# Kernel tuning notes

Measured on AMD Instinct MI355X. Metric: run time of the kernel, lower is better.

The kernel has to match this reference:

```python
import jax, jax.numpy as jnp
import numpy as np

NUM_ATOM_TYPE = 120
NUM_CHIRALITY_TAG = 3
NUM_BOND_TYPE = 6
NUM_BOND_DIRECTION = 3
EMB_DIM = 300
FEAT_DIM = 256
NUM_LAYER = 5
NUM_GRAPHS = 2048
OUT_DIM = 2  # classification: output_dim(1) * 2
BN_EPS = 1e-5


def setup_inputs() -> dict:
    key = jax.random.key(0)
    ks = jax.random.split(key, 20)
    N, E = 100000, 200000
    x = jax.random.randint(ks[0], (N, 2), 0, 3, dtype=jnp.int64) if jax.config.jax_enable_x64 else jax.random.randint(ks[0], (N, 2), 0, 3, dtype=jnp.int32)
    edge_index = jax.random.randint(ks[1], (2, E), 0, N, dtype=x.dtype)
    edge_attr = jax.random.randint(ks[2], (E, 2), 0, 3, dtype=x.dtype)
    batch = jnp.sort(jax.random.randint(ks[3], (N,), 0, NUM_GRAPHS, dtype=x.dtype))
    f32 = jnp.float32
    return {
        'x': x, 'edge_index': edge_index, 'edge_attr': edge_attr, 'batch': batch,
        'x_emb1': jax.random.normal(ks[4], (NUM_ATOM_TYPE, EMB_DIM), f32) * 0.1,
        'x_emb2': jax.random.normal(ks[5], (NUM_CHIRALITY_TAG, EMB_DIM), f32) * 0.1,
        'conv_w': jax.random.normal(ks[6], (NUM_LAYER, EMB_DIM, EMB_DIM), f32) * (1.0 / np.sqrt(EMB_DIM)),
        'conv_b': jnp.zeros((NUM_LAYER, EMB_DIM), f32),
        'eemb1': jax.random.normal(ks[7], (NUM_LAYER, NUM_BOND_TYPE, 1), f32) * 0.1,
        'eemb2': jax.random.normal(ks[8], (NUM_LAYER, NUM_BOND_DIRECTION, 1), f32) * 0.1,
        'bn_gamma': jnp.ones((NUM_LAYER, EMB_DIM), f32),
        'bn_beta': jnp.zeros((NUM_LAYER, EMB_DIM), f32),
        'feat_w': jax.random.normal(ks[9], (EMB_DIM, FEAT_DIM), f32) * (1.0 / np.sqrt(EMB_DIM)),
        'feat_b': jnp.zeros((FEAT_DIM,), f32),
        'pred_w1': jax.random.normal(ks[10], (FEAT_DIM, FEAT_DIM // 2), f32) * (1.0 / np.sqrt(FEAT_DIM)),
        'pred_b1': jnp.zeros((FEAT_DIM // 2,), f32),
        'pred_w2': jax.random.normal(ks[11], (FEAT_DIM // 2, OUT_DIM), f32) * (1.0 / np.sqrt(FEAT_DIM // 2)),
        'pred_b2': jnp.zeros((OUT_DIM,), f32),
    }


def reference(x, edge_index, edge_attr, batch, x_emb1, x_emb2, conv_w, conv_b,
              eemb1, eemb2, bn_gamma, bn_beta, feat_w, feat_b,
              pred_w1, pred_b1, pred_w2, pred_b2):
    N = x.shape[0]
    # add self loops (same for every layer)
    loop = jnp.arange(N, dtype=edge_index.dtype)
    src = jnp.concatenate([edge_index[0], loop])            # [E+N]
    dst = jnp.concatenate([edge_index[1], loop])            # [E+N]
    # self-loop edge attr: bond type 4, direction 0
    ea0 = jnp.concatenate([edge_attr[:, 0], jnp.full((N,), 4, edge_attr.dtype)])
    ea1 = jnp.concatenate([edge_attr[:, 1], jnp.zeros((N,), edge_attr.dtype)])

    h = x_emb1[x[:, 0]] + x_emb2[x[:, 1]]                   # [N, emb_dim]
    for l in range(NUM_LAYER):
        e = eemb1[l][ea0] + eemb2[l][ea1]                   # [E+N, 1]
        hw = h @ conv_w[l]                                  # [N, emb_dim]
        msg = hw[src] + e                                   # gather + broadcast-add
        out = jax.ops.segment_sum(msg, dst, num_segments=N) + conv_b[l]
        # BatchNorm1d (training-mode batch stats, biased variance)
        mean = jnp.mean(out, axis=0)
        var = jnp.mean((out - mean) ** 2, axis=0)
        out = (out - mean) * jax.lax.rsqrt(var + BN_EPS) * bn_gamma[l] + bn_beta[l]
        h = jax.nn.relu(out)                                # dropout p=0

    h = h @ feat_w + feat_b                                 # [N, feat_dim]
    # global mean pool per graph
    sums = jax.ops.segment_sum(h, batch, num_segments=NUM_GRAPHS)
    counts = jax.ops.segment_sum(jnp.ones((N,), h.dtype), batch, num_segments=NUM_GRAPHS)
    g = sums / jnp.maximum(counts, 1.0)[:, None]            # [G, feat_dim]
    pred = jax.nn.relu(g @ pred_w1 + pred_b1) @ pred_w2 + pred_b2
    return (g, pred)
```

## Files before the change

### kernel.cpp

```cpp
#include <hip/hip_runtime.h>
#include <math.h>

#define EMB 300
#define KP 320
#define FEAT 256
#define NLAYER 5
#define NGRAPH 2048
#define BNEPS 1e-5f
#define SCAN_B 256
#define NPART 64
#define CH 40
#define CHW 20

typedef __attribute__((ext_vector_type(8))) short short8;
typedef __attribute__((ext_vector_type(8))) unsigned short ushort8;
typedef __attribute__((ext_vector_type(4))) float f32x4;

#define GLOAD_LDS16(src, dst) __builtin_amdgcn_global_load_lds( \
    (const __attribute__((address_space(1))) unsigned int*)(const void*)(src), \
    (__attribute__((address_space(3))) unsigned int*)(void*)(dst), 16, 0, 0)

static __device__ __forceinline__ unsigned short f2bf(float f) {
    unsigned int u = __float_as_uint(f);
    unsigned int r = (u + 0x7FFFu + ((u >> 16) & 1u)) >> 16;
    return (unsigned short)r;
}
static __device__ __forceinline__ float bf2f(unsigned short h) {
    return __uint_as_float(((unsigned int)h) << 16);
}

__global__ void k_prepW(const float* __restrict__ convw, const float* __restrict__ featw,
                        unsigned short* __restrict__ whi) {
    int idx = blockIdx.x * 256 + threadIdx.x;
    if (idx >= 1856 * KP) return;
    int row = idx / KP;
    int k = idx - row * KP;
    float w = 0.f;
    if (row < 1600) {
        int l = row / KP;
        int c = row - l * KP;
        if (c < EMB && k < EMB) w = convw[(size_t)l * EMB * EMB + (size_t)k * EMB + c];
    } else {
        int c = row - 1600;
        if (k < EMB) w = featw[(size_t)k * FEAT + c];
    }
    whi[idx] = f2bf(w);
}

__global__ void k_s_all(const int* __restrict__ ei, const int* __restrict__ ea,
                        const float* __restrict__ eemb1, const float* __restrict__ eemb2,
                        float* __restrict__ s, int N, int E) {
    int t = blockIdx.x * blockDim.x + threadIdx.x;
    int total = E + N;
    if (t >= total) return;
    if (t < E) {
        int d = ei[E + t];
        int a0 = ea[2 * t], a1 = ea[2 * t + 1];
        for (int l = 0; l < NLAYER; ++l) {
            float v = eemb1[l * 6 + a0] + eemb2[l * 3 + a1];
            atomicAdd(&s[(size_t)l * N + d], v);
        }
    } else {
        int v = t - E;
        for (int l = 0; l < NLAYER; ++l) {
            float val = eemb1[l * 6 + 4] + eemb2[l * 3 + 0];
            atomicAdd(&s[(size_t)l * N + v], val);
        }
    }
}

__global__ void k_count(const int* __restrict__ ei, int* __restrict__ deg, int E) {
    int e = blockIdx.x * blockDim.x + threadIdx.x;
    if (e < E) atomicAdd(&deg[ei[E + e]], 1);
}

__global__ void k_scanA(const int* __restrict__ deg, int* __restrict__ bsum, int N) {
    __shared__ int sm[SCAN_B];
    int i = blockIdx.x * SCAN_B + threadIdx.x;
    sm[threadIdx.x] = (i < N) ? deg[i] : 0;
    __syncthreads();
    for (int off = SCAN_B / 2; off > 0; off >>= 1) {
        if (threadIdx.x < off) sm[threadIdx.x] += sm[threadIdx.x + off];
        __syncthreads();
    }
    if (threadIdx.x == 0) bsum[blockIdx.x] = sm[0];
}

__global__ void k_scanB(int* __restrict__ bsum, int nb, int* __restrict__ rowptr, int N) {
    if (threadIdx.x == 0 && blockIdx.x == 0) {
        int acc = 0;
        for (int i = 0; i < nb; ++i) { int v = bsum[i]; bsum[i] = acc; acc += v; }
        rowptr[N] = acc;
    }
}

__global__ void k_scanC(const int* __restrict__ deg, const int* __restrict__ bsum,
                        int* __restrict__ rowptr, int N) {
    __shared__ int sm[SCAN_B];
    int i = blockIdx.x * SCAN_B + threadIdx.x;
    int v = (i < N) ? deg[i] : 0;
    sm[threadIdx.x] = v;
    __syncthreads();
    for (int off = 1; off < SCAN_B; off <<= 1) {
        int add = (threadIdx.x >= off) ? sm[threadIdx.x - off] : 0;
        __syncthreads();
        sm[threadIdx.x] += add;
        __syncthreads();
    }
    if (i < N) rowptr[i] = bsum[blockIdx.x] + sm[threadIdx.x] - v;
}

__global__ void k_scatter(const int* __restrict__ ei, const int* __restrict__ rowptr,
                          int* __restrict__ cursor, int* __restrict__ esrc, int E) {
    int e = blockIdx.x * blockDim.x + threadIdx.x;
    if (e >= E) return;
    int d = ei[E + e], srcv = ei[e];
    int p = atomicAdd(&cursor[d], 1);
    esrc[rowptr[d] + p] = srcv;
}

__global__ void k_h0(const int* __restrict__ x, const float* __restrict__ emb1,
                     const float* __restrict__ emb2, unsigned short* __restrict__ h0, int N) {
    int idx = blockIdx.x * 256 + threadIdx.x;
    if (idx >= N * 160) return;
    int v = idx / 160, fp = idx - v * 160;
    unsigned int out = 0;
    if (fp < 150) {
        int f = fp * 2;
        size_t b1 = (size_t)x[2 * v] * EMB + f;
        size_t b2 = (size_t)x[2 * v + 1] * EMB + f;
        float a = emb1[b1] + emb2[b2];
        float b = emb1[b1 + 1] + emb2[b2 + 1];
        out = (unsigned int)f2bf(a) | ((unsigned int)f2bf(b) << 16);
    }
    *(unsigned int*)(h0 + (size_t)v * KP + fp * 2) = out;
}

template <bool BN>
__global__ __launch_bounds__(256) void k_aggV(
    const unsigned short* __restrict__ Prev, const int* __restrict__ rowptr,
    const int* __restrict__ esrc,
    const float* __restrict__ scale, const float* __restrict__ shift,
    unsigned short* __restrict__ A, int N) {
    int idx = blockIdx.x * 256 + threadIdx.x;
    if (idx >= N * CHW) return;
    int row = idx / CHW, c = idx - row * CHW;
    int f0 = c * 16;

    f32x4 sc[4], sh[4];
    if constexpr (BN) {
#pragma unroll
        for (int g = 0; g < 4; ++g) {
            sc[g] = *(const f32x4*)(scale + f0 + g * 4);
            sh[g] = *(const f32x4*)(shift + f0 + g * 4);
        }
    }
    int rs = rowptr[row], re = rowptr[row + 1];

    float f[16];
    {
        const unsigned short* pr = Prev + (size_t)row * KP + f0;
        ushort8 u0 = *(const ushort8*)pr;
        ushort8 u1 = *(const ushort8*)(pr + 8);
#pragma unroll
        for (int e = 0; e < 8; ++e) {
            if constexpr (BN) {
                f[e]     = fmaxf(fmaf(bf2f(u0[e]), sc[e >> 2][e & 3], sh[e >> 2][e & 3]), 0.f);
                f[e + 8] = fmaxf(fmaf(bf2f(u1[e]), sc[2 + (e >> 2)][e & 3], sh[2 + (e >> 2)][e & 3]), 0.f);
            } else {
                f[e] = bf2f(u0[e]);
                f[e + 8] = bf2f(u1[e]);
            }
        }
    }
    int ii = rs;
    int un = (ii < re) ? esrc[ii] : 0;
    while (ii < re) {
        int ucur = un;
        ++ii;
        if (ii < re) un = esrc[ii];
        const unsigned short* pu = Prev + (size_t)ucur * KP + f0;
        ushort8 uu0 = *(const ushort8*)pu;
        ushort8 uu1 = *(const ushort8*)(pu + 8);
#pragma unroll
        for (int e = 0; e < 8; ++e) {
            if constexpr (BN) {
                f[e]     += fmaxf(fmaf(bf2f(uu0[e]), sc[e >> 2][e & 3], sh[e >> 2][e & 3]), 0.f);
                f[e + 8] += fmaxf(fmaf(bf2f(uu1[e]), sc[2 + (e >> 2)][e & 3], sh[2 + (e >> 2)][e & 3]), 0.f);
            } else {
                f[e] += bf2f(uu0[e]);
                f[e + 8] += bf2f(uu1[e]);
            }
        }
    }
    short8 v0, v1;
#pragma unroll
    for (int e = 0; e < 8; ++e) {
        v0[e] = (short)f2bf(f[e]);
        v1[e] = (short)f2bf(f[e + 8]);
    }
    unsigned short* dst = A + (size_t)row * KP + f0;
    *(short8*)dst = v0;
    *(short8*)(dst + 8) = v1;
}

template <int COLF, int BMT, bool BN>
__global__ __launch_bounds__(256, 2) void k_mm(
    const unsigned short* __restrict__ Prev,
    const float* __restrict__ scale, const float* __restrict__ shift,
    const unsigned short* __restrict__ Whi,
    const float* __restrict__ bias, const float* __restrict__ svec,
    unsigned short* __restrict__ OutB,
    float* __restrict__ partsum, float* __restrict__ partsq, int N) {
    __shared__ unsigned short As[BMT * KP];
    constexpr int WSTR = (COLF == 5) ? KP : FEAT;
    constexpr int RF = BMT / 16;
    constexpr int NCHUNK = BMT * CH;
    int tid = threadIdx.x;
    int row0 = blockIdx.x * BMT;
    int wave = tid >> 6, lane = tid & 63;

    if constexpr (!BN) {
#pragma unroll
        for (int it = 0; it < NCHUNK / 256; ++it) {
            int base = it * 256 + wave * 64;
            int idx = base + lane;
            int r = idx / CH, c = idx - r * CH;
            const unsigned short* src =
                Prev + (size_t)(row0 + r) * KP + (size_t)(c ^ (r & 7)) * 8;
            GLOAD_LDS16(src, &As[(size_t)base * 8]);
        }
    } else {
        for (int idx = tid; idx < NCHUNK; idx += 256) {
            int r = idx / CH, c = idx - r * CH;
            int row = row0 + r;
            short8 v = (short8){0, 0, 0, 0, 0, 0, 0, 0};
            if (row < N) {
                ushort8 u = *(const ushort8*)(Prev + (size_t)row * KP + c * 8);
                f32x4 s0 = *(const f32x4*)(scale + c * 8);
                f32x4 s1 = *(const f32x4*)(scale + c * 8 + 4);
                f32x4 t0 = *(const f32x4*)(shift + c * 8);
                f32x4 t1 = *(const f32x4*)(shift + c * 8 + 4);
#pragma unroll
                for (int e = 0; e < 4; ++e) {
                    v[e]     = (short)f2bf(fmaxf(fmaf(bf2f(u[e]), s0[e], t0[e]), 0.f));
                    v[e + 4] = (short)f2bf(fmaxf(fmaf(bf2f(u[e + 4]), s1[e], t1[e]), 0.f));
                }
            }
            *(short8*)&As[(size_t)(r * CH + (c ^ (r & 7))) * 8] = v;
        }
    }
    __syncthreads();

    int q = lane >> 4, m = lane & 15;
    int wbase = wave * (COLF * 16);

    f32x4 acc[RF][COLF];
#pragma unroll
    for (int rf = 0; rf < RF; ++rf)
#pragma unroll
        for (int cf = 0; cf < COLF; ++cf)
            acc[rf][cf] = (f32x4){0.f, 0.f, 0.f, 0.f};

    size_t woff[COLF];
#pragma unroll
    for (int cf = 0; cf < COLF; ++cf)
        woff[cf] = (size_t)(wbase + cf * 16 + m) * KP;

#pragma unroll 2
    for (int ks = 0; ks < 10; ++ks) {
        short8 a[RF];
#pragma unroll
        for (int rf = 0; rf < RF; ++rf) {
            int r = rf * 16 + m;
            int ch = ks * 4 + q;
            a[rf] = *(const short8*)&As[(size_t)(r * CH + (ch ^ (r & 7))) * 8];
        }
        int kb = ks * 32 + q * 8;
#pragma unroll
        for (int cf = 0; cf < COLF; ++cf) {
            short8 bh = *(const short8*)(Whi + woff[cf] + kb);
#pragma unroll
            for (int rf = 0; rf < RF; ++rf) {
                acc[rf][cf] = __builtin_amdgcn_mfma_f32_16x16x32_bf16(a[rf], bh, acc[rf][cf], 0, 0, 0);
            }
        }
    }

    __syncthreads();

    if constexpr (COLF == 5) {
        float sv[RF][4];
#pragma unroll
        for (int rf = 0; rf < RF; ++rf)
#pragma unroll
            for (int i = 0; i < 4; ++i) {
                int row = row0 + rf * 16 + q * 4 + i;
                sv[rf][i] = (row < N) ? svec[row] : 0.f;
            }
        int part = blockIdx.x & (NPART - 1);
#pragma unroll
        for (int cf = 0; cf < COLF; ++cf) {
            int col = wbase + cf * 16 + m;
            bool cok = col < EMB;
            float bia = cok ? bias[col] : 0.f;
            float lsum = 0.f, lsq = 0.f;
#pragma unroll
            for (int rf = 0; rf < RF; ++rf)
#pragma unroll
                for (int i = 0; i < 4; ++i) {
                    int r = rf * 16 + q * 4 + i;
                    int row = row0 + r;
                    float val = 0.f;
                    if (cok && row < N) {
                        val = acc[rf][cf][i] + bia + sv[rf][i];
                        lsum += val; lsq += val * val;
                    }
                    As[(size_t)r * WSTR + col] = f2bf(val);
                }
            lsum += __shfl_xor(lsum, 16); lsum += __shfl_xor(lsum, 32);
            lsq  += __shfl_xor(lsq, 16);  lsq  += __shfl_xor(lsq, 32);
            if (q == 0 && cok) {
                atomicAdd(&partsum[(size_t)part * KP + col], lsum);
                atomicAdd(&partsq[(size_t)part * KP + col], lsq);
            }
        }
    } else {
#pragma unroll
        for (int cf = 0; cf < COLF; ++cf) {
            int col = wbase + cf * 16 + m;
            float bia = bias[col];
#pragma unroll
            for (int rf = 0; rf < RF; ++rf)
#pragma unroll
                for (int i = 0; i < 4; ++i) {
                    int r = rf * 16 + q * 4 + i;
                    As[(size_t)r * WSTR + col] = f2bf(acc[rf][cf][i] + bia);
                }
        }
    }
    __syncthreads();

    unsigned short* dst = OutB + (size_t)row0 * WSTR;
    for (int idx = tid; idx < BMT * WSTR / 8; idx += 256) {
        *(short8*)(dst + (size_t)idx * 8) = *(const short8*)&As[(size_t)idx * 8];
    }
}

__global__ __launch_bounds__(64) void k_bnred(
    const float* __restrict__ partsum, const float* __restrict__ partsq,
    const float* __restrict__ gamma, const float* __restrict__ beta,
    float* __restrict__ scale, float* __restrict__ shift, int N) {
    int j = blockIdx.x;
    int p = threadIdx.x;
    if (j >= EMB) {
        if (p == 0) { scale[j] = 0.f; shift[j] = 0.f; }
        return;
    }
    float s = partsum[(size_t)p * KP + j];
    float sq = partsq[(size_t)p * KP + j];
#pragma unroll
    for (int off = 32; off > 0; off >>= 1) {
        s += __shfl_down(s, off);
        sq += __shfl_down(sq, off);
    }
    if (p == 0) {
        float invN = 1.0f / (float)N;
        float mean = s * invN;
        float var = sq * invN - mean * mean;
        float sc = gamma[j] * rsqrtf(var + BNEPS);
        scale[j] = sc;
        shift[j] = beta[j] - mean * sc;
    }
}

__global__ void k_counts(const int* __restrict__ batch, float* __restrict__ counts, int N) {
    int i = blockIdx.x * blockDim.x + threadIdx.x;
    if (i < N) atomicAdd(&counts[batch[i]], 1.0f);
}

#define PROWS 128
__global__ __launch_bounds__(256) void k_pool(const unsigned short* __restrict__ H,
                                              const int* __restrict__ batch,
                                              float* __restrict__ gsums, int N) {
    int j = threadIdx.x;
    int r0 = blockIdx.x * PROWS;
    int rend = min(r0 + PROWS, N);
    float run = 0.f;
    int curg = -1;
    for (int r = r0; r < rend; ++r) {
        int g = batch[r];
        if (g != curg) {
            if (curg >= 0) atomicAdd(&gsums[(size_t)curg * FEAT + j], run);
            curg = g; run = 0.f;
        }
        run += bf2f(H[(size_t)r * FEAT + j]);
    }
    if (curg >= 0) atomicAdd(&gsums[(size_t)curg * FEAT + j], run);
}

__global__ void k_poolfin(const float* __restrict__ gsums, const float* __restrict__ counts,
                          float* __restrict__ gout) {
    int i = blockIdx.x * blockDim.x + threadIdx.x;
    if (i >= NGRAPH * FEAT) return;
    int g = i / FEAT;
    gout[i] = gsums[i] / fmaxf(counts[g], 1.0f);
}

__global__ __launch_bounds__(128) void k_pred(
    const float* __restrict__ gout, const float* __restrict__ w1, const float* __restrict__ b1,
    const float* __restrict__ w2, const float* __restrict__ b2, float* __restrict__ pout) {
    __shared__ float gs[FEAT];
    __shared__ float h1[128];
    int g = blockIdx.x;
    for (int k = threadIdx.x; k < FEAT; k += 128) gs[k] = gout[(size_t)g * FEAT + k];
    __syncthreads();
    int j = threadIdx.x;
    float acc = b1[j];
    for (int k = 0; k < FEAT; ++k) acc = fmaf(gs[k], w1[(size_t)k * 128 + j], acc);
    h1[j] = fmaxf(acc, 0.f);
    __syncthreads();
    if (j < 2) {
        float acc2 = b2[j];
        for (int k = 0; k < 128; ++k) acc2 = fmaf(h1[k], w2[k * 2 + j], acc2);
        pout[(size_t)g * 2 + j] = acc2;
    }
}

extern "C" void kernel_launch(void* const* d_in, const int* in_sizes, int n_in,
                              void* d_out, int out_size, void* d_ws, size_t ws_size,
                              hipStream_t stream) {
    const int* x      = (const int*)d_in[0];
    const int* ei     = (const int*)d_in[1];
    const int* ea     = (const int*)d_in[2];
    const int* batch  = (const int*)d_in[3];
    const float* xemb1 = (const float*)d_in[4];
    const float* xemb2 = (const float*)d_in[5];
    const float* convw = (const float*)d_in[6];
    const float* convb = (const float*)d_in[7];
    const float* eemb1 = (const float*)d_in[8];
    const float* eemb2 = (const float*)d_in[9];
    const float* gamma = (const float*)d_in[10];
    const float* beta  = (const float*)d_in[11];
    const float* featw = (const float*)d_in[12];
    const float* featb = (const float*)d_in[13];
    const float* pw1   = (const float*)d_in[14];
    const float* pb1   = (const float*)d_in[15];
    const float* pw2   = (const float*)d_in[16];
    const float* pb2   = (const float*)d_in[17];

    int N = in_sizes[0] / 2;
    int E = in_sizes[1] / 2;
    int nrb = (N + 127) / 128;
    size_t Npad = (size_t)nrb * 128;

    char* p = (char*)d_ws;
    auto alloc = [&](size_t bytes) { char* r = p; p += (bytes + 255) & ~255ull; return r; };
    unsigned short* H0Hf = (unsigned short*)alloc(Npad * KP * 2);
    unsigned short* Abf  = (unsigned short*)alloc(Npad * KP * 2);
    unsigned short* OutB = (unsigned short*)alloc(Npad * KP * 2);
    float* sAll    = (float*)alloc((size_t)NLAYER * N * 4);
    float* partsum = (float*)alloc((size_t)NLAYER * NPART * KP * 4);
    float* partsq  = (float*)alloc((size_t)NLAYER * NPART * KP * 4);
    char*  zero1_end = p;
    float* scaleA  = (float*)alloc((size_t)NLAYER * KP * 4);
    float* shiftA  = (float*)alloc((size_t)NLAYER * KP * 4);
    unsigned short* Whi = (unsigned short*)alloc((size_t)1856 * KP * 2);
    int*   deg    = (int*)alloc((size_t)N * 4);
    int*   rowptr = (int*)alloc((size_t)(N + 1) * 4);
    int*   cursor = (int*)alloc((size_t)N * 4);
    char*  zero2_end = p;
    int*   esrc   = (int*)alloc((size_t)E * 4);
    float* gsums  = (float*)alloc((size_t)NGRAPH * FEAT * 4);
    float* counts = (float*)alloc(NGRAPH * 4);
    char*  zero3_end = p;
    int nb = (N + SCAN_B - 1) / SCAN_B;
    int*   bsum   = (int*)alloc((size_t)nb * 4);

    hipMemsetAsync(sAll, 0, (size_t)(zero1_end - (char*)sAll), stream);
    hipMemsetAsync(deg, 0, (size_t)(zero2_end - (char*)deg), stream);
    hipMemsetAsync(gsums, 0, (size_t)(zero3_end - (char*)gsums), stream);
    if (Npad > (size_t)N)
        hipMemsetAsync(Abf + (size_t)N * KP, 0, (Npad - (size_t)N) * KP * 2, stream);

    int tpb = 256;
    k_prepW<<<(1856 * KP + 255) / 256, 256, 0, stream>>>(convw, featw, Whi);
    k_s_all<<<(E + N + tpb - 1) / tpb, tpb, 0, stream>>>(ei, ea, eemb1, eemb2, sAll, N, E);
    k_count<<<(E + tpb - 1) / tpb, tpb, 0, stream>>>(ei, deg, E);
    k_scanA<<<nb, SCAN_B, 0, stream>>>(deg, bsum, N);
    k_scanB<<<1, 64, 0, stream>>>(bsum, nb, rowptr, N);
    k_scanC<<<nb, SCAN_B, 0, stream>>>(deg, bsum, rowptr, N);
    k_scatter<<<(E + tpb - 1) / tpb, tpb, 0, stream>>>(ei, rowptr, cursor, esrc, E);
    k_h0<<<(N * 160 + 255) / 256, 256, 0, stream>>>(x, xemb1, xemb2, H0Hf, N);

    int gagg = (N * CHW + 255) / 256;
    k_aggV<false><<<gagg, 256, 0, stream>>>(H0Hf, rowptr, esrc, nullptr, nullptr, Abf, N);

    for (int l = 0; l < NLAYER; ++l) {
        k_mm<5, 128, false><<<nrb, 256, 0, stream>>>(
            Abf, nullptr, nullptr,
            Whi + (size_t)l * KP * KP,
            convb + (size_t)l * EMB, sAll + (size_t)l * N,
            OutB,
            partsum + (size_t)l * NPART * KP, partsq + (size_t)l * NPART * KP, N);
        k_bnred<<<KP, 64, 0, stream>>>(
            partsum + (size_t)l * NPART * KP, partsq + (size_t)l * NPART * KP,
            gamma + (size_t)l * EMB, beta + (size_t)l * EMB,
            scaleA + (size_t)l * KP, shiftA + (size_t)l * KP, N);
        if (l < NLAYER - 1)
            k_aggV<true><<<gagg, 256, 0, stream>>>(OutB, rowptr, esrc,
                                                   scaleA + (size_t)l * KP, shiftA + (size_t)l * KP,
                                                   Abf, N);
    }

    k_mm<4, 128, true><<<nrb, 256, 0, stream>>>(
        OutB, scaleA + (size_t)4 * KP, shiftA + (size_t)4 * KP,
        Whi + (size_t)1600 * KP,
        featb, nullptr,
        H0Hf, nullptr, nullptr, N);

    float* gout = (float*)d_out;
    float* pout = gout + (size_t)NGRAPH * FEAT;
    k_counts<<<(N + tpb - 1) / tpb, tpb, 0, stream>>>(batch, counts, N);
    k_pool<<<(N + PROWS - 1) / PROWS, 256, 0, stream>>>(H0Hf, batch, gsums, N);
    k_poolfin<<<(NGRAPH * FEAT + tpb - 1) / tpb, tpb, 0, stream>>>(gsums, counts, gout);
    k_pred<<<NGRAPH, 128, 0, stream>>>(gout, pw1, pb1, pw2, pb2, pout);
}
```

Before: 811.0 us.

## Replace per-layer edge-embedding atomics with attribute histogram and fold pooling kernels

Measured after the change: 745.7 us. -8.0%, faster.

```diff
diff --git a/kernel.cpp b/kernel.cpp
--- a/kernel.cpp
+++ b/kernel.cpp
@@ -47,25 +47,30 @@
     whi[idx] = f2bf(w);
 }
 
-__global__ void k_s_all(const int* __restrict__ ei, const int* __restrict__ ea,
-                        const float* __restrict__ eemb1, const float* __restrict__ eemb2,
-                        float* __restrict__ s, int N, int E) {
-    int t = blockIdx.x * blockDim.x + threadIdx.x;
-    int total = E + N;
-    if (t >= total) return;
-    if (t < E) {
-        int d = ei[E + t];
-        int a0 = ea[2 * t], a1 = ea[2 * t + 1];
-        for (int l = 0; l < NLAYER; ++l) {
-            float v = eemb1[l * 6 + a0] + eemb2[l * 3 + a1];
-            atomicAdd(&s[(size_t)l * N + d], v);
-        }
-    } else {
-        int v = t - E;
-        for (int l = 0; l < NLAYER; ++l) {
-            float val = eemb1[l * 6 + 4] + eemb2[l * 3 + 0];
-            atomicAdd(&s[(size_t)l * N + v], val);
-        }
+__global__ void k_hist(const int* __restrict__ ei, const int* __restrict__ ea,
+                       int* __restrict__ hist, int E) {
+    int e = blockIdx.x * 256 + threadIdx.x;
+    if (e >= E) return;
+    int d = ei[E + e];
+    atomicAdd(&hist[(size_t)d * 12 + ea[2 * e]], 1);
+    atomicAdd(&hist[(size_t)d * 12 + 6 + ea[2 * e + 1]], 1);
+}
+
+__global__ void k_sexp(const int* __restrict__ hist, const float* __restrict__ eemb1,
+                       const float* __restrict__ eemb2, float* __restrict__ s, int N) {
+    int v = blockIdx.x * 256 + threadIdx.x;
+    if (v >= N) return;
+    int h[12];
+#pragma unroll
+    for (int k = 0; k < 12; ++k) h[k] = hist[(size_t)v * 12 + k];
+#pragma unroll
+    for (int l = 0; l < NLAYER; ++l) {
+        float acc = eemb1[l * 6 + 4] + eemb2[l * 3 + 0];
+#pragma unroll
+        for (int k = 0; k < 6; ++k) acc += (float)h[k] * eemb1[l * 6 + k];
+#pragma unroll
+        for (int k = 0; k < 3; ++k) acc += (float)h[6 + k] * eemb2[l * 3 + k];
+        s[(size_t)l * N + v] = acc;
     }
 }
 
@@ -374,46 +379,49 @@
     }
 }
 
-__global__ void k_counts(const int* __restrict__ batch, float* __restrict__ counts, int N) {
-    int i = blockIdx.x * blockDim.x + threadIdx.x;
-    if (i < N) atomicAdd(&counts[batch[i]], 1.0f);
-}
-
 #define PROWS 128
 __global__ __launch_bounds__(256) void k_pool(const unsigned short* __restrict__ H,
                                               const int* __restrict__ batch,
-                                              float* __restrict__ gsums, int N) {
+                                              float* __restrict__ gsums,
+                                              float* __restrict__ counts, int N) {
     int j = threadIdx.x;
     int r0 = blockIdx.x * PROWS;
     int rend = min(r0 + PROWS, N);
     float run = 0.f;
+    int runlen = 0;
     int curg = -1;
     for (int r = r0; r < rend; ++r) {
         int g = batch[r];
         if (g != curg) {
-            if (curg >= 0) atomicAdd(&gsums[(size_t)curg * FEAT + j], run);
-            curg = g; run = 0.f;
+            if (curg >= 0) {
+                atomicAdd(&gsums[(size_t)curg * FEAT + j], run);
+                if (j == 0) atomicAdd(&counts[curg], (float)runlen);
+            }
+            curg = g; run = 0.f; runlen = 0;
         }
         run += bf2f(H[(size_t)r * FEAT + j]);
-    }
-    if (curg >= 0) atomicAdd(&gsums[(size_t)curg * FEAT + j], run);
-}
-
-__global__ void k_poolfin(const float* __restrict__ gsums, const float* __restrict__ counts,
-                          float* __restrict__ gout) {
-    int i = blockIdx.x * blockDim.x + threadIdx.x;
-    if (i >= NGRAPH * FEAT) return;
-    int g = i / FEAT;
-    gout[i] = gsums[i] / fmaxf(counts[g], 1.0f);
+        ++runlen;
+    }
+    if (curg >= 0) {
+        atomicAdd(&gsums[(size_t)curg * FEAT + j], run);
+        if (j == 0) atomicAdd(&counts[curg], (float)runlen);
+    }
 }
 
 __global__ __launch_bounds__(128) void k_pred(
-    const float* __restrict__ gout, const float* __restrict__ w1, const float* __restrict__ b1,
-    const float* __restrict__ w2, const float* __restrict__ b2, float* __restrict__ pout) {
+    const float* __restrict__ gsums, const float* __restrict__ counts,
+    const float* __restrict__ w1, const float* __restrict__ b1,
+    const float* __restrict__ w2, const float* __restrict__ b2,
+    float* __restrict__ gout, float* __restrict__ pout) {
     __shared__ float gs[FEAT];
     __shared__ float h1[128];
     int g = blockIdx.x;
-    for (int k = threadIdx.x; k < FEAT; k += 128) gs[k] = gout[(size_t)g * FEAT + k];
+    float invc = 1.0f / fmaxf(counts[g], 1.0f);
+    for (int k = threadIdx.x; k < FEAT; k += 128) {
+        float val = gsums[(size_t)g * FEAT + k] * invc;
+        gs[k] = val;
+        gout[(size_t)g * FEAT + k] = val;
+    }
     __syncthreads();
     int j = threadIdx.x;
     float acc = b1[j];
@@ -459,16 +467,17 @@
     unsigned short* H0Hf = (unsigned short*)alloc(Npad * KP * 2);
     unsigned short* Abf  = (unsigned short*)alloc(Npad * KP * 2);
     unsigned short* OutB = (unsigned short*)alloc(Npad * KP * 2);
-    float* sAll    = (float*)alloc((size_t)NLAYER * N * 4);
     float* partsum = (float*)alloc((size_t)NLAYER * NPART * KP * 4);
     float* partsq  = (float*)alloc((size_t)NLAYER * NPART * KP * 4);
     char*  zero1_end = p;
+    float* sAll    = (float*)alloc((size_t)NLAYER * N * 4);
     float* scaleA  = (float*)alloc((size_t)NLAYER * KP * 4);
     float* shiftA  = (float*)alloc((size_t)NLAYER * KP * 4);
     unsigned short* Whi = (unsigned short*)alloc((size_t)1856 * KP * 2);
     int*   deg    = (int*)alloc((size_t)N * 4);
     int*   rowptr = (int*)alloc((size_t)(N + 1) * 4);
     int*   cursor = (int*)alloc((size_t)N * 4);
+    int*   hist   = (int*)alloc((size_t)N * 12 * 4);
     char*  zero2_end = p;
     int*   esrc   = (int*)alloc((size_t)E * 4);
     float* gsums  = (float*)alloc((size_t)NGRAPH * FEAT * 4);
@@ -477,7 +486,7 @@
     int nb = (N + SCAN_B - 1) / SCAN_B;
     int*   bsum   = (int*)alloc((size_t)nb * 4);
 
-    hipMemsetAsync(sAll, 0, (size_t)(zero1_end - (char*)sAll), stream);
+    hipMemsetAsync(partsum, 0, (size_t)(zero1_end - (char*)partsum), stream);
     hipMemsetAsync(deg, 0, (size_t)(zero2_end - (char*)deg), stream);
     hipMemsetAsync(gsums, 0, (size_t)(zero3_end - (char*)gsums), stream);
     if (Npad > (size_t)N)
@@ -485,7 +494,8 @@
 
     int tpb = 256;
     k_prepW<<<(1856 * KP + 255) / 256, 256, 0, stream>>>(convw, featw, Whi);
-    k_s_all<<<(E + N + tpb - 1) / tpb, tpb, 0, stream>>>(ei, ea, eemb1, eemb2, sAll, N, E);
+    k_hist<<<(E + 255) / 256, 256, 0, stream>>>(ei, ea, hist, E);
+    k_sexp<<<(N + 255) / 256, 256, 0, stream>>>(hist, eemb1, eemb2, sAll, N);
     k_count<<<(E + tpb - 1) / tpb, tpb, 0, stream>>>(ei, deg, E);
     k_scanA<<<nb, SCAN_B, 0, stream>>>(deg, bsum, N);
     k_scanB<<<1, 64, 0, stream>>>(bsum, nb, rowptr, N);
@@ -521,8 +531,6 @@
 
     float* gout = (float*)d_out;
     float* pout = gout + (size_t)NGRAPH * FEAT;
-    k_counts<<<(N + tpb - 1) / tpb, tpb, 0, stream>>>(batch, counts, N);
-    k_pool<<<(N + PROWS - 1) / PROWS, 256, 0, stream>>>(H0Hf, batch, gsums, N);
-    k_poolfin<<<(NGRAPH * FEAT + tpb - 1) / tpb, tpb, 0, stream>>>(gsums, counts, gout);
-    k_pred<<<NGRAPH, 128, 0, stream>>>(gout, pw1, pb1, pw2, pb2, pout);
-}
+    k_pool<<<(N + PROWS - 1) / PROWS, 256, 0, stream>>>(H0Hf, batch, gsums, counts, N);
+    k_pred<<<NGRAPH, 128, 0, stream>>>(gsums, counts, pw1, pb1, pw2, pb2, gout, pout);
+}
```
